# Performance work log

Hardware: AMD Instinct MI355X
Metric: run time of the kernel (lower is better)

Reference implementation:

```python
import jax, jax.numpy as jnp
import numpy as np

NUM_QUANTIZERS = 8


def setup_inputs() -> dict:
    key = jax.random.key(0)
    k1, k2 = jax.random.split(key)
    B, W, C = 16, 2048, 512
    Q, K = NUM_QUANTIZERS, 1024
    x = jax.random.normal(k1, (B, W, C), dtype=jnp.float32)
    # per-stage codebooks (shared_codebook=False), xavier-normal-ish scale
    codebooks = jax.random.normal(k2, (Q, K, C), dtype=jnp.float32) * (2.0 / (K + C)) ** 0.5
    return {"x": x, "codebooks": codebooks}


def reference(x, codebooks):
    """Residual quantization: per-stage cdist+argmin+lookup+residual update.

    x: [B, W, C] encoder latents; codebooks: [Q, K, C].
    Returns (final_z_q [B*W, C], commitment_loss scalar) — final_z_q is
    sum over quantizer stages of the straight-through quantized outputs
    (is_train=True path).
    """
    B, W, C = x.shape
    first_z_e = x.reshape(B * W, C)            # (b w) c
    z_e = first_z_e
    z_d = jnp.zeros_like(first_z_e)
    quant_sum = jnp.zeros_like(first_z_e)
    q_latent = jnp.float32(0.0)
    e_latent = jnp.float32(0.0)
    rq_latent = jnp.float32(0.0)
    for i in range(codebooks.shape[0]):
        cb = codebooks[i]                      # [K, C]
        # squared euclidean distances (argmin-equivalent to torch.cdist)
        dist2 = (jnp.sum(z_e * z_e, axis=1, keepdims=True)
                 - 2.0 * (z_e @ cb.T)
                 + jnp.sum(cb * cb, axis=1))   # [N, K]
        idx = jnp.argmin(dist2, axis=1)        # [N]
        z_q = cb[idx]                          # codebook lookup, [N, C]
        z_d = z_d + jax.lax.stop_gradient(z_q)
        q_latent = q_latent + jnp.mean((jax.lax.stop_gradient(z_e) - z_q) ** 2)
        e_latent = e_latent + jnp.mean((z_e - jax.lax.stop_gradient(z_q)) ** 2)
        rq_latent = rq_latent + jnp.mean((first_z_e - z_d) ** 2)
        # straight-through estimator (is_train=True)
        z_q_st = z_e + jax.lax.stop_gradient(z_q - z_e)
        quant_sum = quant_sum + z_q_st
        z_e = z_e - z_q_st
    commitment_loss = 0.75 * q_latent + e_latent + rq_latent
    return quant_sum, commitment_loss
```

## Files before the change

kernel.cpp:

```cpp
#include <hip/hip_runtime.h>

#define N_ROWS 32768
#define C_DIM  512
#define K_CODES 1024
#define Q_STAGES 8

typedef __attribute__((ext_vector_type(8))) short bf16x8;
typedef __attribute__((ext_vector_type(4))) float f32x4;
typedef __attribute__((ext_vector_type(4))) unsigned short u16x4;
typedef __attribute__((ext_vector_type(8))) unsigned short u16x8;

#define ZEH_OFF 0ull
#define ZEL_OFF 33554432ull
#define CBH_OFF 67108864ull
#define CBL_OFF 68157440ull
#define C2_OFF  69206016ull
#define IDX_OFF 69238784ull
#define RPT_OFF 69304320ull

#define GLD(gp, lp) __builtin_amdgcn_global_load_lds( \
    (const __attribute__((address_space(1))) void*)(gp), \
    (__attribute__((address_space(3))) void*)(lp), 16, 0, 0)

__device__ __forceinline__ float bf_hi_f(float f) {
    return __uint_as_float(__float_as_uint(f) & 0xFFFF0000u);
}
__device__ __forceinline__ unsigned short bf_hi_u(float f) {
    return (unsigned short)(__float_as_uint(f) >> 16);
}
__device__ __forceinline__ float u2f(unsigned short u) {
    return __uint_as_float(((unsigned int)u) << 16);
}

__global__ __launch_bounds__(256) void split_kernel(
    const float* __restrict__ src, unsigned short* __restrict__ h,
    unsigned short* __restrict__ l, int n4)
{
    int i = blockIdx.x * 256 + threadIdx.x;
    if (i >= n4) return;
    float4 v = *(const float4*)(src + (size_t)i * 4);
    u16x4 hv, lv;
    float f, hf;
    f = v.x; hv[0] = bf_hi_u(f); hf = bf_hi_f(f); lv[0] = bf_hi_u(f - hf);
    f = v.y; hv[1] = bf_hi_u(f); hf = bf_hi_f(f); lv[1] = bf_hi_u(f - hf);
    f = v.z; hv[2] = bf_hi_u(f); hf = bf_hi_f(f); lv[2] = bf_hi_u(f - hf);
    f = v.w; hv[3] = bf_hi_u(f); hf = bf_hi_f(f); lv[3] = bf_hi_u(f - hf);
    *(u16x4*)(h + (size_t)i * 4) = hv;
    *(u16x4*)(l + (size_t)i * 4) = lv;
}

__global__ __launch_bounds__(256) void rowsq_kernel(
    const float* __restrict__ src, float* __restrict__ dst, int nrows)
{
    int wave = (blockIdx.x * blockDim.x + threadIdx.x) >> 6;
    int lane = threadIdx.x & 63;
    if (wave >= nrows) return;
    const float* p = src + (size_t)wave * C_DIM + lane * 8;
    float4 a = *(const float4*)p;
    float4 b = *(const float4*)(p + 4);
    float s = a.x*a.x + a.y*a.y + a.z*a.z + a.w*a.w
            + b.x*b.x + b.y*b.y + b.z*b.z + b.w*b.w;
    #pragma unroll
    for (int off = 1; off < 64; off <<= 1) s += __shfl_xor(s, off);
    if (lane == 0) dst[wave] = s;
}

#define DBM2 128
#define DBNC 256
#define DBK 32
#define NSTEPS 64

__global__ __launch_bounds__(512, 2) void dist_kernel(
    const unsigned short* __restrict__ zeh, const unsigned short* __restrict__ zel,
    const unsigned short* __restrict__ cbh, const unsigned short* __restrict__ cbl,
    const float* __restrict__ c2s, unsigned short* __restrict__ idx_out)
{
    __shared__ unsigned short sA[3][2][DBM2 * DBK];
    __shared__ unsigned short sB[3][2][DBNC * DBK];
    __shared__ float c2_lds[K_CODES];

    const int tid  = threadIdx.x;
    const int lane = tid & 63;
    const int w    = tid >> 6;
    const int wr   = w >> 2;
    const int wc   = w & 3;
    const int lr   = lane & 15;
    const int kg   = lane >> 4;
    const int row0 = blockIdx.x * DBM2;

    for (int i = tid; i < K_CODES; i += 512) c2_lds[i] = c2s[i];

    const int srow = lane >> 2;
    const int scol = (((lane & 3) ^ ((srow >> 1) & 3))) * 8;
    const int aslot = (kg ^ ((lr >> 1) & 3)) * 8;

    float rbv[4][4];
    int   rbi[4][4];
    #pragma unroll
    for (int i = 0; i < 4; ++i)
        #pragma unroll
        for (int r = 0; r < 4; ++r) { rbv[i][r] = 3.4e38f; rbi[i][r] = 0x7fffffff; }

    f32x4 acc[4][4];
    #pragma unroll
    for (int i = 0; i < 4; ++i)
        #pragma unroll
        for (int j = 0; j < 4; ++j) acc[i][j] = (f32x4)0.f;

    auto stage = [&](int t, int b) {
        const int col0 = (t >> 4) * DBNC;
        const int kk = (t & 15) * DBK;
        GLD(zeh + (size_t)(row0 + w * 16 + srow) * C_DIM + kk + scol,
            &sA[b][0][(w * 16) * DBK]);
        GLD(zel + (size_t)(row0 + w * 16 + srow) * C_DIM + kk + scol,
            &sA[b][1][(w * 16) * DBK]);
        #pragma unroll
        for (int u = 0; u < 2; ++u) {
            const int rB = w * 32 + u * 16;
            GLD(cbh + (size_t)(col0 + rB + srow) * C_DIM + kk + scol,
                &sB[b][0][rB * DBK]);
            GLD(cbl + (size_t)(col0 + rB + srow) * C_DIM + kk + scol,
                &sB[b][1][rB * DBK]);
        }
    };

    __syncthreads();
    stage(0, 0);
    stage(1, 1);

    int cur = 0;
    #pragma unroll 1
    for (int t = 0; t < NSTEPS; ++t) {
        if (t == NSTEPS - 1) {
            asm volatile("s_waitcnt vmcnt(0)" ::: "memory");
        } else {
            asm volatile("s_waitcnt vmcnt(6)" ::: "memory");
        }
        __builtin_amdgcn_s_barrier();

        bf16x8 ah[4], al[4], bh[4], bl[4];
        #pragma unroll
        for (int mi = 0; mi < 4; ++mi) {
            const int rowoff = (wr * 64 + mi * 16 + lr) * DBK + aslot;
            ah[mi] = *(const bf16x8*)&sA[cur][0][rowoff];
            al[mi] = *(const bf16x8*)&sA[cur][1][rowoff];
        }
        #pragma unroll
        for (int ni = 0; ni < 4; ++ni) {
            const int rowoff = (wc * 64 + ni * 16 + lr) * DBK + aslot;
            bh[ni] = *(const bf16x8*)&sB[cur][0][rowoff];
            bl[ni] = *(const bf16x8*)&sB[cur][1][rowoff];
        }

        if (t < NSTEPS - 2) {
            int nxt = cur + 2; if (nxt > 2) nxt -= 3;
            stage(t + 2, nxt);
        }

        __builtin_amdgcn_s_setprio(1);
        #pragma unroll
        for (int mi = 0; mi < 4; ++mi)
            #pragma unroll
            for (int ni = 0; ni < 4; ++ni)
                acc[mi][ni] = __builtin_amdgcn_mfma_f32_16x16x32_bf16(
                    ah[mi], bh[ni], acc[mi][ni], 0, 0, 0);
        #pragma unroll
        for (int mi = 0; mi < 4; ++mi)
            #pragma unroll
            for (int ni = 0; ni < 4; ++ni)
                acc[mi][ni] = __builtin_amdgcn_mfma_f32_16x16x32_bf16(
                    ah[mi], bl[ni], acc[mi][ni], 0, 0, 0);
        #pragma unroll
        for (int mi = 0; mi < 4; ++mi)
            #pragma unroll
            for (int ni = 0; ni < 4; ++ni)
                acc[mi][ni] = __builtin_amdgcn_mfma_f32_16x16x32_bf16(
                    al[mi], bh[ni], acc[mi][ni], 0, 0, 0);
        __builtin_amdgcn_s_setprio(0);

        if ((t & 15) == 15) {
            const int col0 = (t >> 4) * DBNC;
            #pragma unroll
            for (int ni = 0; ni < 4; ++ni) {
                const int code = col0 + wc * 64 + ni * 16 + lr;
                const float c2v = c2_lds[code];
                #pragma unroll
                for (int mi = 0; mi < 4; ++mi)
                    #pragma unroll
                    for (int r = 0; r < 4; ++r) {
                        float d = fmaf(-2.f, acc[mi][ni][r], c2v);
                        if (d < rbv[mi][r]) { rbv[mi][r] = d; rbi[mi][r] = code; }
                    }
            }
            #pragma unroll
            for (int i = 0; i < 4; ++i)
                #pragma unroll
                for (int j = 0; j < 4; ++j) acc[i][j] = (f32x4)0.f;
        }

        cur = (cur == 2) ? 0 : cur + 1;
    }

    #pragma unroll
    for (int off = 1; off < 16; off <<= 1) {
        #pragma unroll
        for (int mi = 0; mi < 4; ++mi)
            #pragma unroll
            for (int r = 0; r < 4; ++r) {
                float ov = __shfl_xor(rbv[mi][r], off);
                int   oi = __shfl_xor(rbi[mi][r], off);
                if (ov < rbv[mi][r] || (ov == rbv[mi][r] && oi < rbi[mi][r])) {
                    rbv[mi][r] = ov; rbi[mi][r] = oi;
                }
            }
    }

    __syncthreads();
    float (*s_v)[4] = (float (*)[4])&sA[0][0][0];
    int   (*s_i)[4] = (int (*)[4])((char*)&sA[0][0][0] + DBM2 * 4 * 4);
    if (lr == 0) {
        #pragma unroll
        for (int mi = 0; mi < 4; ++mi)
            #pragma unroll
            for (int r = 0; r < 4; ++r) {
                int lrow = wr * 64 + mi * 16 + kg * 4 + r;
                s_v[lrow][wc] = rbv[mi][r];
                s_i[lrow][wc] = rbi[mi][r];
            }
    }
    __syncthreads();
    if (tid < DBM2) {
        float bv = s_v[tid][0]; int bi = s_i[tid][0];
        #pragma unroll
        for (int c = 1; c < 4; ++c) {
            float v = s_v[tid][c]; int i = s_i[tid][c];
            if (v < bv || (v == bv && i < bi)) { bv = v; bi = i; }
        }
        idx_out[row0 + tid] = (unsigned short)bi;
    }
}

__global__ __launch_bounds__(1024) void update_kernel(
    const int s, const float* __restrict__ x, const float* __restrict__ cb,
    const float* __restrict__ cb_next, const unsigned short* __restrict__ idx_sel,
    float* __restrict__ out, unsigned short* __restrict__ zeh,
    unsigned short* __restrict__ zel, unsigned short* __restrict__ cbh,
    unsigned short* __restrict__ cbl, float* __restrict__ rpart)
{
    if (blockIdx.x >= 2048) {
        int i = (blockIdx.x - 2048) * 1024 + threadIdx.x;
        float4 v = *(const float4*)(cb_next + (size_t)i * 4);
        u16x4 hv, lv;
        float f, hf;
        f = v.x; hv[0] = bf_hi_u(f); hf = bf_hi_f(f); lv[0] = bf_hi_u(f - hf);
        f = v.y; hv[1] = bf_hi_u(f); hf = bf_hi_f(f); lv[1] = bf_hi_u(f - hf);
        f = v.z; hv[2] = bf_hi_u(f); hf = bf_hi_f(f); lv[2] = bf_hi_u(f - hf);
        f = v.w; hv[3] = bf_hi_u(f); hf = bf_hi_f(f); lv[3] = bf_hi_u(f - hf);
        *(u16x4*)(cbh + (size_t)i * 4) = hv;
        *(u16x4*)(cbl + (size_t)i * 4) = lv;
        return;
    }

    __shared__ float swsum[16];
    const int wid = threadIdx.x >> 6, lane = threadIdx.x & 63;
    const int r = blockIdx.x * 16 + wid;
    const int bi = idx_sel[r];
    const size_t base = (size_t)r * C_DIM + lane * 8;
    const float* q = cb + (size_t)bi * C_DIM + lane * 8;

    float4 q0 = *(const float4*)q;
    float4 q1 = *(const float4*)(q + 4);
    float qq[8] = {q0.x, q0.y, q0.z, q0.w, q1.x, q1.y, q1.z, q1.w};

    float v[8];
    if (s == 0) {
        float4 z0 = *(const float4*)(x + base);
        float4 z1 = *(const float4*)(x + base + 4);
        v[0]=z0.x; v[1]=z0.y; v[2]=z0.z; v[3]=z0.w;
        v[4]=z1.x; v[5]=z1.y; v[6]=z1.z; v[7]=z1.w;
    } else {
        u16x8 h = *(const u16x8*)(zeh + base);
        u16x8 l = *(const u16x8*)(zel + base);
        #pragma unroll
        for (int j = 0; j < 8; ++j) v[j] = u2f(h[j]) + u2f(l[j]);
    }

    float rr[8];
    #pragma unroll
    for (int j = 0; j < 8; ++j) rr[j] = v[j] - qq[j];

    if (s < Q_STAGES - 1) {
        u16x8 hh, ll;
        #pragma unroll
        for (int j = 0; j < 8; ++j) {
            hh[j] = bf_hi_u(rr[j]);
            float lo = rr[j] - bf_hi_f(rr[j]);
            ll[j] = bf_hi_u(lo);
        }
        *(u16x8*)(zeh + base) = hh;
        *(u16x8*)(zel + base) = ll;
    } else {
        float4 x0 = *(const float4*)(x + base);
        float4 x1 = *(const float4*)(x + base + 4);
        float4 o0, o1;
        o0.x = x0.x - rr[0]; o0.y = x0.y - rr[1];
        o0.z = x0.z - rr[2]; o0.w = x0.w - rr[3];
        o1.x = x1.x - rr[4]; o1.y = x1.y - rr[5];
        o1.z = x1.z - rr[6]; o1.w = x1.w - rr[7];
        *(float4*)(out + base)     = o0;
        *(float4*)(out + base + 4) = o1;
    }

    float ssum = 0.f;
    #pragma unroll
    for (int j = 0; j < 8; ++j) ssum += rr[j] * rr[j];
    #pragma unroll
    for (int off = 1; off < 64; off <<= 1) ssum += __shfl_xor(ssum, off);
    if (lane == 0) swsum[wid] = ssum;
    __syncthreads();
    if (threadIdx.x == 0) {
        float t = 0.f;
        #pragma unroll
        for (int i = 0; i < 16; ++i) t += swsum[i];
        rpart[blockIdx.x] = t;
    }
}

__global__ __launch_bounds__(1024) void finalize_all_kernel(
    const float* __restrict__ rpart, float* __restrict__ out_loss)
{
    __shared__ float sm[1024];
    const int t = threadIdx.x;
    float tot = 0.f;
    for (int s = 0; s < Q_STAGES; ++s) {
        sm[t] = rpart[s * 2048 + t] + rpart[s * 2048 + 1024 + t];
        __syncthreads();
        for (int w2 = 512; w2 > 0; w2 >>= 1) {
            if (t < w2) sm[t] += sm[t + w2];
            __syncthreads();
        }
        if (t == 0) tot += sm[0];
        __syncthreads();
    }
    if (t == 0) out_loss[0] = 2.75f * tot / (float)((size_t)N_ROWS * C_DIM);
}

extern "C" void kernel_launch(void* const* d_in, const int* in_sizes, int n_in,
                              void* d_out, int out_size, void* d_ws, size_t ws_size,
                              hipStream_t stream)
{
    const float* x   = (const float*)d_in[0];
    const float* cbs = (const float*)d_in[1];
    float* out = (float*)d_out;
    char* ws = (char*)d_ws;

    unsigned short* zeh = (unsigned short*)(ws + ZEH_OFF);
    unsigned short* zel = (unsigned short*)(ws + ZEL_OFF);
    unsigned short* cbh = (unsigned short*)(ws + CBH_OFF);
    unsigned short* cbl = (unsigned short*)(ws + CBL_OFF);
    float* c2    = (float*)(ws + C2_OFF);
    unsigned short* gidx = (unsigned short*)(ws + IDX_OFF);
    float* rpart = (float*)(ws + RPT_OFF);

    split_kernel<<<(N_ROWS * C_DIM / 4 + 255) / 256, 256, 0, stream>>>(
        x, zeh, zel, N_ROWS * C_DIM / 4);
    split_kernel<<<(K_CODES * C_DIM / 4 + 255) / 256, 256, 0, stream>>>(
        cbs, cbh, cbl, K_CODES * C_DIM / 4);
    rowsq_kernel<<<(Q_STAGES * K_CODES * 64) / 256, 256, 0, stream>>>(
        cbs, c2, Q_STAGES * K_CODES);

    for (int s = 0; s < Q_STAGES; ++s) {
        const float* cb  = cbs + (size_t)s * K_CODES * C_DIM;
        const float* cbn = (s < Q_STAGES - 1) ? cb + (size_t)K_CODES * C_DIM : cbs;
        dist_kernel<<<N_ROWS / DBM2, 512, 0, stream>>>(
            zeh, zel, cbh, cbl, c2 + (size_t)s * K_CODES, gidx);
        const int nblk = (s < Q_STAGES - 1) ? 2048 + 128 : 2048;
        update_kernel<<<nblk, 1024, 0, stream>>>(
            s, x, cb, cbn, gidx, out, zeh, zel, cbh, cbl, rpart + s * 2048);
    }
    finalize_all_kernel<<<1, 1024, 0, stream>>>(rpart, out + (size_t)N_ROWS * C_DIM);
}
```

Baseline: 988.2 us.

## Load codebook fragments straight into registers and double-buffer the latent tiles

The codebook (B operand) tile no longer goes through LDS. Each wave loads its own MFMA B fragments directly from global memory into double-buffered registers, one step ahead. The latent (A) tile now uses two LDS buffers with a one-step prefetch instead of three buffers with a two-step prefetch. This removes LDS traffic and footprint for B, but waves sharing a column slice load the same codebook data twice. It also relies on short-row strided global reads and only one step of latency hiding.

Measured after the change: 1.503 ms. +52.1%, slower.

```diff
diff --git a/kernel.cpp b/kernel.cpp
--- a/kernel.cpp
+++ b/kernel.cpp
@@ -70,13 +70,87 @@
 #define DBK 32
 #define NSTEPS 64
 
+#define STAGE_A(t, b) do {                                                  \
+    const int kk_ = ((t) & 15) * DBK;                                       \
+    GLD(zeh + (size_t)(row0 + w * 16 + srow) * C_DIM + kk_ + scol,          \
+        &sA[b][0][(w * 16) * DBK]);                                         \
+    GLD(zel + (size_t)(row0 + w * 16 + srow) * C_DIM + kk_ + scol,          \
+        &sA[b][1][(w * 16) * DBK]);                                         \
+} while (0)
+
+#define LOAD_B(t, bh_, bl_) do {                                            \
+    const size_t o_ = bofs + (size_t)((t) >> 4) * (DBNC * C_DIM)            \
+                    + ((t) & 15) * DBK;                                     \
+    _Pragma("unroll")                                                       \
+    for (int ni_ = 0; ni_ < 4; ++ni_) {                                     \
+        bh_[ni_] = *(const bf16x8*)(cbh + o_ + ni_ * 16 * C_DIM);           \
+        bl_[ni_] = *(const bf16x8*)(cbl + o_ + ni_ * 16 * C_DIM);           \
+    }                                                                       \
+} while (0)
+
+#define STEP(t, ab, bhC, blC, bhN, blN) do {                                \
+    asm volatile("s_waitcnt vmcnt(8)" ::: "memory");                        \
+    __builtin_amdgcn_s_barrier();                                           \
+    bf16x8 ah_[4], al_[4];                                                  \
+    _Pragma("unroll")                                                       \
+    for (int mi_ = 0; mi_ < 4; ++mi_) {                                     \
+        const int ro_ = (wr * 64 + mi_ * 16 + lr) * DBK + aslot;            \
+        ah_[mi_] = *(const bf16x8*)&sA[ab][0][ro_];                         \
+        al_[mi_] = *(const bf16x8*)&sA[ab][1][ro_];                         \
+    }                                                                       \
+    if ((t) < NSTEPS - 1) {                                                 \
+        STAGE_A((t) + 1, (ab) ^ 1);                                         \
+        LOAD_B((t) + 1, bhN, blN);                                          \
+    }                                                                       \
+    __builtin_amdgcn_s_setprio(1);                                          \
+    _Pragma("unroll")                                                       \
+    for (int mi_ = 0; mi_ < 4; ++mi_)                                       \
+        _Pragma("unroll")                                                   \
+        for (int ni_ = 0; ni_ < 4; ++ni_)                                   \
+            acc[mi_][ni_] = __builtin_amdgcn_mfma_f32_16x16x32_bf16(        \
+                ah_[mi_], bhC[ni_], acc[mi_][ni_], 0, 0, 0);                \
+    _Pragma("unroll")                                                       \
+    for (int mi_ = 0; mi_ < 4; ++mi_)                                       \
+        _Pragma("unroll")                                                   \
+        for (int ni_ = 0; ni_ < 4; ++ni_)                                   \
+            acc[mi_][ni_] = __builtin_amdgcn_mfma_f32_16x16x32_bf16(        \
+                ah_[mi_], blC[ni_], acc[mi_][ni_], 0, 0, 0);                \
+    _Pragma("unroll")                                                       \
+    for (int mi_ = 0; mi_ < 4; ++mi_)                                       \
+        _Pragma("unroll")                                                   \
+        for (int ni_ = 0; ni_ < 4; ++ni_)                                   \
+            acc[mi_][ni_] = __builtin_amdgcn_mfma_f32_16x16x32_bf16(        \
+                al_[mi_], bhC[ni_], acc[mi_][ni_], 0, 0, 0);                \
+    __builtin_amdgcn_s_setprio(0);                                          \
+    if (((t) & 15) == 15) {                                                 \
+        const int col0_ = ((t) >> 4) * DBNC;                                \
+        _Pragma("unroll")                                                   \
+        for (int ni_ = 0; ni_ < 4; ++ni_) {                                 \
+            const int code_ = col0_ + wc * 64 + ni_ * 16 + lr;              \
+            const float c2v_ = c2_lds[code_];                               \
+            _Pragma("unroll")                                               \
+            for (int mi_ = 0; mi_ < 4; ++mi_)                               \
+                _Pragma("unroll")                                           \
+                for (int r_ = 0; r_ < 4; ++r_) {                            \
+                    float d_ = fmaf(-2.f, acc[mi_][ni_][r_], c2v_);         \
+                    if (d_ < rbv[mi_][r_]) {                                \
+                        rbv[mi_][r_] = d_; rbi[mi_][r_] = code_;            \
+                    }                                                       \
+                }                                                           \
+        }                                                                   \
+        _Pragma("unroll")                                                   \
+        for (int i_ = 0; i_ < 4; ++i_)                                      \
+            _Pragma("unroll")                                               \
+            for (int j_ = 0; j_ < 4; ++j_) acc[i_][j_] = (f32x4)0.f;        \
+    }                                                                       \
+} while (0)
+
 __global__ __launch_bounds__(512, 2) void dist_kernel(
     const unsigned short* __restrict__ zeh, const unsigned short* __restrict__ zel,
     const unsigned short* __restrict__ cbh, const unsigned short* __restrict__ cbl,
     const float* __restrict__ c2s, unsigned short* __restrict__ idx_out)
 {
-    __shared__ unsigned short sA[3][2][DBM2 * DBK];
-    __shared__ unsigned short sB[3][2][DBNC * DBK];
+    __shared__ unsigned short sA[2][2][DBM2 * DBK];
     __shared__ float c2_lds[K_CODES];
 
     const int tid  = threadIdx.x;
@@ -94,6 +168,8 @@
     const int scol = (((lane & 3) ^ ((srow >> 1) & 3))) * 8;
     const int aslot = (kg ^ ((lr >> 1) & 3)) * 8;
 
+    const size_t bofs = (size_t)(wc * 64 + lr) * C_DIM + kg * 8;
+
     float rbv[4][4];
     int   rbi[4][4];
     #pragma unroll
@@ -107,98 +183,17 @@
         #pragma unroll
         for (int j = 0; j < 4; ++j) acc[i][j] = (f32x4)0.f;
 
-    auto stage = [&](int t, int b) {
-        const int col0 = (t >> 4) * DBNC;
-        const int kk = (t & 15) * DBK;
-        GLD(zeh + (size_t)(row0 + w * 16 + srow) * C_DIM + kk + scol,
-            &sA[b][0][(w * 16) * DBK]);
-        GLD(zel + (size_t)(row0 + w * 16 + srow) * C_DIM + kk + scol,
-            &sA[b][1][(w * 16) * DBK]);
-        #pragma unroll
-        for (int u = 0; u < 2; ++u) {
-            const int rB = w * 32 + u * 16;
-            GLD(cbh + (size_t)(col0 + rB + srow) * C_DIM + kk + scol,
-                &sB[b][0][rB * DBK]);
-            GLD(cbl + (size_t)(col0 + rB + srow) * C_DIM + kk + scol,
-                &sB[b][1][rB * DBK]);
-        }
-    };
-
     __syncthreads();
-    stage(0, 0);
-    stage(1, 1);
-
-    int cur = 0;
+
+    STAGE_A(0, 0);
+    bf16x8 bhA[4], blA[4], bhB[4], blB[4];
+    LOAD_B(0, bhA, blA);
+
     #pragma unroll 1
-    for (int t = 0; t < NSTEPS; ++t) {
-        if (t == NSTEPS - 1) {
-            asm volatile("s_waitcnt vmcnt(0)" ::: "memory");
-        } else {
-            asm volatile("s_waitcnt vmcnt(6)" ::: "memory");
-        }
-        __builtin_amdgcn_s_barrier();
-
-        bf16x8 ah[4], al[4], bh[4], bl[4];
-        #pragma unroll
-        for (int mi = 0; mi < 4; ++mi) {
-            const int rowoff = (wr * 64 + mi * 16 + lr) * DBK + aslot;
-            ah[mi] = *(const bf16x8*)&sA[cur][0][rowoff];
-            al[mi] = *(const bf16x8*)&sA[cur][1][rowoff];
-        }
-        #pragma unroll
-        for (int ni = 0; ni < 4; ++ni) {
-            const int rowoff = (wc * 64 + ni * 16 + lr) * DBK + aslot;
-            bh[ni] = *(const bf16x8*)&sB[cur][0][rowoff];
-            bl[ni] = *(const bf16x8*)&sB[cur][1][rowoff];
-        }
-
-        if (t < NSTEPS - 2) {
-            int nxt = cur + 2; if (nxt > 2) nxt -= 3;
-            stage(t + 2, nxt);
-        }
-
-        __builtin_amdgcn_s_setprio(1);
-        #pragma unroll
-        for (int mi = 0; mi < 4; ++mi)
-            #pragma unroll
-            for (int ni = 0; ni < 4; ++ni)
-                acc[mi][ni] = __builtin_amdgcn_mfma_f32_16x16x32_bf16(
-                    ah[mi], bh[ni], acc[mi][ni], 0, 0, 0);
-        #pragma unroll
-        for (int mi = 0; mi < 4; ++mi)
-            #pragma unroll
-            for (int ni = 0; ni < 4; ++ni)
-                acc[mi][ni] = __builtin_amdgcn_mfma_f32_16x16x32_bf16(
-                    ah[mi], bl[ni], acc[mi][ni], 0, 0, 0);
-        #pragma unroll
-        for (int mi = 0; mi < 4; ++mi)
-            #pragma unroll
-            for (int ni = 0; ni < 4; ++ni)
-                acc[mi][ni] = __builtin_amdgcn_mfma_f32_16x16x32_bf16(
-                    al[mi], bh[ni], acc[mi][ni], 0, 0, 0);
-        __builtin_amdgcn_s_setprio(0);
-
-        if ((t & 15) == 15) {
-            const int col0 = (t >> 4) * DBNC;
-            #pragma unroll
-            for (int ni = 0; ni < 4; ++ni) {
-                const int code = col0 + wc * 64 + ni * 16 + lr;
-                const float c2v = c2_lds[code];
-                #pragma unroll
-                for (int mi = 0; mi < 4; ++mi)
-                    #pragma unroll
-                    for (int r = 0; r < 4; ++r) {
-                        float d = fmaf(-2.f, acc[mi][ni][r], c2v);
-                        if (d < rbv[mi][r]) { rbv[mi][r] = d; rbi[mi][r] = code; }
-                    }
-            }
-            #pragma unroll
-            for (int i = 0; i < 4; ++i)
-                #pragma unroll
-                for (int j = 0; j < 4; ++j) acc[i][j] = (f32x4)0.f;
-        }
-
-        cur = (cur == 2) ? 0 : cur + 1;
+    for (int i = 0; i < NSTEPS / 2; ++i) {
+        const int t0 = 2 * i;
+        STEP(t0,     0, bhA, blA, bhB, blB);
+        STEP(t0 + 1, 1, bhB, blB, bhA, blA);
     }
 
     #pragma unroll
```

## Widen dist kernel code tile to 512 and switch to double buffering

Applied to the files above, without the earlier changes.

The distance GEMM's code-column tile doubles from 256 to 512, so each wave holds a 4x8 accumulator tile and the K loop runs half as many steps. The staging pipeline drops from triple to double buffering with a full vmcnt(0) wait each step. The B operand hi/lo fragments are loaded in two phases to limit register use, and c2 is read straight from global memory instead of LDS. The intent is more MFMA work per LDS byte and fewer passes over z_e. The risks are much higher register pressure (128 accumulator floats) under launch_bounds(512,2), possible spills, and less latency hiding from the shallower pipeline.

Result: slower. 1.082 ms (+9.5%).

```diff
diff --git a/kernel.cpp b/kernel.cpp
--- a/kernel.cpp
+++ b/kernel.cpp
@@ -66,18 +66,17 @@
 }
 
 #define DBM2 128
-#define DBNC 256
+#define DBNC2 512
 #define DBK 32
-#define NSTEPS 64
+#define NSTEPS 32
 
 __global__ __launch_bounds__(512, 2) void dist_kernel(
     const unsigned short* __restrict__ zeh, const unsigned short* __restrict__ zel,
     const unsigned short* __restrict__ cbh, const unsigned short* __restrict__ cbl,
     const float* __restrict__ c2s, unsigned short* __restrict__ idx_out)
 {
-    __shared__ unsigned short sA[3][2][DBM2 * DBK];
-    __shared__ unsigned short sB[3][2][DBNC * DBK];
-    __shared__ float c2_lds[K_CODES];
+    __shared__ unsigned short sA[2][2][DBM2 * DBK];
+    __shared__ unsigned short sB[2][2][DBNC2 * DBK];
 
     const int tid  = threadIdx.x;
     const int lane = tid & 63;
@@ -88,8 +87,6 @@
     const int kg   = lane >> 4;
     const int row0 = blockIdx.x * DBM2;
 
-    for (int i = tid; i < K_CODES; i += 512) c2_lds[i] = c2s[i];
-
     const int srow = lane >> 2;
     const int scol = (((lane & 3) ^ ((srow >> 1) & 3))) * 8;
     const int aslot = (kg ^ ((lr >> 1) & 3)) * 8;
@@ -101,22 +98,22 @@
         #pragma unroll
         for (int r = 0; r < 4; ++r) { rbv[i][r] = 3.4e38f; rbi[i][r] = 0x7fffffff; }
 
-    f32x4 acc[4][4];
+    f32x4 acc[4][8];
     #pragma unroll
     for (int i = 0; i < 4; ++i)
         #pragma unroll
-        for (int j = 0; j < 4; ++j) acc[i][j] = (f32x4)0.f;
+        for (int j = 0; j < 8; ++j) acc[i][j] = (f32x4)0.f;
 
     auto stage = [&](int t, int b) {
-        const int col0 = (t >> 4) * DBNC;
+        const int col0 = (t >> 4) * DBNC2;
         const int kk = (t & 15) * DBK;
         GLD(zeh + (size_t)(row0 + w * 16 + srow) * C_DIM + kk + scol,
             &sA[b][0][(w * 16) * DBK]);
         GLD(zel + (size_t)(row0 + w * 16 + srow) * C_DIM + kk + scol,
             &sA[b][1][(w * 16) * DBK]);
         #pragma unroll
-        for (int u = 0; u < 2; ++u) {
-            const int rB = w * 32 + u * 16;
+        for (int u = 0; u < 4; ++u) {
+            const int rB = w * 64 + u * 16;
             GLD(cbh + (size_t)(col0 + rB + srow) * C_DIM + kk + scol,
                 &sB[b][0][rB * DBK]);
             GLD(cbl + (size_t)(col0 + rB + srow) * C_DIM + kk + scol,
@@ -124,66 +121,65 @@
         }
     };
 
-    __syncthreads();
     stage(0, 0);
-    stage(1, 1);
-
-    int cur = 0;
+
     #pragma unroll 1
     for (int t = 0; t < NSTEPS; ++t) {
-        if (t == NSTEPS - 1) {
-            asm volatile("s_waitcnt vmcnt(0)" ::: "memory");
-        } else {
-            asm volatile("s_waitcnt vmcnt(6)" ::: "memory");
-        }
+        const int cur = t & 1;
+        asm volatile("s_waitcnt vmcnt(0)" ::: "memory");
         __builtin_amdgcn_s_barrier();
 
-        bf16x8 ah[4], al[4], bh[4], bl[4];
+        if (t < NSTEPS - 1) stage(t + 1, cur ^ 1);
+
+        bf16x8 ah[4], al[4], bx[8];
         #pragma unroll
         for (int mi = 0; mi < 4; ++mi) {
-            const int rowoff = (wr * 64 + mi * 16 + lr) * DBK + aslot;
-            ah[mi] = *(const bf16x8*)&sA[cur][0][rowoff];
-            al[mi] = *(const bf16x8*)&sA[cur][1][rowoff];
-        }
-        #pragma unroll
-        for (int ni = 0; ni < 4; ++ni) {
-            const int rowoff = (wc * 64 + ni * 16 + lr) * DBK + aslot;
-            bh[ni] = *(const bf16x8*)&sB[cur][0][rowoff];
-            bl[ni] = *(const bf16x8*)&sB[cur][1][rowoff];
-        }
-
-        if (t < NSTEPS - 2) {
-            int nxt = cur + 2; if (nxt > 2) nxt -= 3;
-            stage(t + 2, nxt);
+            const int ro = (wr * 64 + mi * 16 + lr) * DBK + aslot;
+            ah[mi] = *(const bf16x8*)&sA[cur][0][ro];
+            al[mi] = *(const bf16x8*)&sA[cur][1][ro];
+        }
+        #pragma unroll
+        for (int ni = 0; ni < 8; ++ni) {
+            const int ro = (wc * 128 + ni * 16 + lr) * DBK + aslot;
+            bx[ni] = *(const bf16x8*)&sB[cur][0][ro];
         }
 
         __builtin_amdgcn_s_setprio(1);
         #pragma unroll
         for (int mi = 0; mi < 4; ++mi)
             #pragma unroll
-            for (int ni = 0; ni < 4; ++ni)
+            for (int ni = 0; ni < 8; ++ni)
                 acc[mi][ni] = __builtin_amdgcn_mfma_f32_16x16x32_bf16(
-                    ah[mi], bh[ni], acc[mi][ni], 0, 0, 0);
-        #pragma unroll
-        for (int mi = 0; mi < 4; ++mi)
-            #pragma unroll
-            for (int ni = 0; ni < 4; ++ni)
+                    ah[mi], bx[ni], acc[mi][ni], 0, 0, 0);
+        #pragma unroll
+        for (int mi = 0; mi < 4; ++mi)
+            #pragma unroll
+            for (int ni = 0; ni < 8; ++ni)
                 acc[mi][ni] = __builtin_amdgcn_mfma_f32_16x16x32_bf16(
-                    ah[mi], bl[ni], acc[mi][ni], 0, 0, 0);
-        #pragma unroll
-        for (int mi = 0; mi < 4; ++mi)
-            #pragma unroll
-            for (int ni = 0; ni < 4; ++ni)
+                    al[mi], bx[ni], acc[mi][ni], 0, 0, 0);
+        __builtin_amdgcn_s_setprio(0);
+
+        #pragma unroll
+        for (int ni = 0; ni < 8; ++ni) {
+            const int ro = (wc * 128 + ni * 16 + lr) * DBK + aslot;
+            bx[ni] = *(const bf16x8*)&sB[cur][1][ro];
+        }
+
+        __builtin_amdgcn_s_setprio(1);
+        #pragma unroll
+        for (int mi = 0; mi < 4; ++mi)
+            #pragma unroll
+            for (int ni = 0; ni < 8; ++ni)
                 acc[mi][ni] = __builtin_amdgcn_mfma_f32_16x16x32_bf16(
-                    al[mi], bh[ni], acc[mi][ni], 0, 0, 0);
+                    ah[mi], bx[ni], acc[mi][ni], 0, 0, 0);
         __builtin_amdgcn_s_setprio(0);
 
         if ((t & 15) == 15) {
-            const int col0 = (t >> 4) * DBNC;
-            #pragma unroll
-            for (int ni = 0; ni < 4; ++ni) {
-                const int code = col0 + wc * 64 + ni * 16 + lr;
-                const float c2v = c2_lds[code];
+            const int col0 = (t >> 4) * DBNC2;
+            #pragma unroll
+            for (int ni = 0; ni < 8; ++ni) {
+                const int code = col0 + wc * 128 + ni * 16 + lr;
+                const float c2v = c2s[code];
                 #pragma unroll
                 for (int mi = 0; mi < 4; ++mi)
                     #pragma unroll
@@ -195,10 +191,8 @@
             #pragma unroll
             for (int i = 0; i < 4; ++i)
                 #pragma unroll
-                for (int j = 0; j < 4; ++j) acc[i][j] = (f32x4)0.f;
-        }
-
-        cur = (cur == 2) ? 0 : cur + 1;
+                for (int j = 0; j < 8; ++j) acc[i][j] = (f32x4)0.f;
+        }
     }
 
     #pragma unroll
```

## Shrink distance tile to 64 rows with 4 waves and double buffering

Applied to the files above, without the earlier changes.

The distance GEMM block goes from 128x256 with 8 waves and triple-buffered LDS to 64x256 with 4 waves and double buffering. The prefetch is issued right after the barrier with a full vmcnt(0) wait, and the per-block c2 LDS preload is dropped in favour of reading c2 from global memory during the argmin epilogue. This halves the LDS footprint per block and doubles the grid size, which may allow more concurrent blocks. In exchange, codebook tiles are reused across half as many rows, so codebook global traffic doubles, and the shallower pipeline exposes more load latency.

Result: slower. 1.139 ms (+15.2%).

```diff
diff --git a/kernel.cpp b/kernel.cpp
--- a/kernel.cpp
+++ b/kernel.cpp
@@ -65,30 +65,25 @@
     if (lane == 0) dst[wave] = s;
 }
 
-#define DBM2 128
+#define DBM3 64
 #define DBNC 256
 #define DBK 32
 #define NSTEPS 64
 
-__global__ __launch_bounds__(512, 2) void dist_kernel(
+__global__ __launch_bounds__(256, 2) void dist_kernel(
     const unsigned short* __restrict__ zeh, const unsigned short* __restrict__ zel,
     const unsigned short* __restrict__ cbh, const unsigned short* __restrict__ cbl,
     const float* __restrict__ c2s, unsigned short* __restrict__ idx_out)
 {
-    __shared__ unsigned short sA[3][2][DBM2 * DBK];
-    __shared__ unsigned short sB[3][2][DBNC * DBK];
-    __shared__ float c2_lds[K_CODES];
+    __shared__ unsigned short sA[2][2][DBM3 * DBK];
+    __shared__ unsigned short sB[2][2][DBNC * DBK];
 
     const int tid  = threadIdx.x;
     const int lane = tid & 63;
     const int w    = tid >> 6;
-    const int wr   = w >> 2;
-    const int wc   = w & 3;
     const int lr   = lane & 15;
     const int kg   = lane >> 4;
-    const int row0 = blockIdx.x * DBM2;
-
-    for (int i = tid; i < K_CODES; i += 512) c2_lds[i] = c2s[i];
+    const int row0 = blockIdx.x * DBM3;
 
     const int srow = lane >> 2;
     const int scol = (((lane & 3) ^ ((srow >> 1) & 3))) * 8;
@@ -115,8 +110,8 @@
         GLD(zel + (size_t)(row0 + w * 16 + srow) * C_DIM + kk + scol,
             &sA[b][1][(w * 16) * DBK]);
         #pragma unroll
-        for (int u = 0; u < 2; ++u) {
-            const int rB = w * 32 + u * 16;
+        for (int u = 0; u < 4; ++u) {
+            const int rB = w * 64 + u * 16;
             GLD(cbh + (size_t)(col0 + rB + srow) * C_DIM + kk + scol,
                 &sB[b][0][rB * DBK]);
             GLD(cbl + (size_t)(col0 + rB + srow) * C_DIM + kk + scol,
@@ -124,37 +119,28 @@
         }
     };
 
-    __syncthreads();
     stage(0, 0);
-    stage(1, 1);
-
-    int cur = 0;
+
     #pragma unroll 1
     for (int t = 0; t < NSTEPS; ++t) {
-        if (t == NSTEPS - 1) {
-            asm volatile("s_waitcnt vmcnt(0)" ::: "memory");
-        } else {
-            asm volatile("s_waitcnt vmcnt(6)" ::: "memory");
-        }
+        const int cur = t & 1;
+        asm volatile("s_waitcnt vmcnt(0)" ::: "memory");
         __builtin_amdgcn_s_barrier();
 
+        if (t < NSTEPS - 1) stage(t + 1, cur ^ 1);
+
         bf16x8 ah[4], al[4], bh[4], bl[4];
         #pragma unroll
         for (int mi = 0; mi < 4; ++mi) {
-            const int rowoff = (wr * 64 + mi * 16 + lr) * DBK + aslot;
-            ah[mi] = *(const bf16x8*)&sA[cur][0][rowoff];
-            al[mi] = *(const bf16x8*)&sA[cur][1][rowoff];
+            const int ro = (mi * 16 + lr) * DBK + aslot;
+            ah[mi] = *(const bf16x8*)&sA[cur][0][ro];
+            al[mi] = *(const bf16x8*)&sA[cur][1][ro];
         }
         #pragma unroll
         for (int ni = 0; ni < 4; ++ni) {
-            const int rowoff = (wc * 64 + ni * 16 + lr) * DBK + aslot;
-            bh[ni] = *(const bf16x8*)&sB[cur][0][rowoff];
-            bl[ni] = *(const bf16x8*)&sB[cur][1][rowoff];
-        }
-
-        if (t < NSTEPS - 2) {
-            int nxt = cur + 2; if (nxt > 2) nxt -= 3;
-            stage(t + 2, nxt);
+            const int ro = (w * 64 + ni * 16 + lr) * DBK + aslot;
+            bh[ni] = *(const bf16x8*)&sB[cur][0][ro];
+            bl[ni] = *(const bf16x8*)&sB[cur][1][ro];
         }
 
         __builtin_amdgcn_s_setprio(1);
@@ -182,8 +168,8 @@
             const int col0 = (t >> 4) * DBNC;
             #pragma unroll
             for (int ni = 0; ni < 4; ++ni) {
-                const int code = col0 + wc * 64 + ni * 16 + lr;
-                const float c2v = c2_lds[code];
+                const int code = col0 + w * 64 + ni * 16 + lr;
+                const float c2v = c2s[code];
                 #pragma unroll
                 for (int mi = 0; mi < 4; ++mi)
                     #pragma unroll
@@ -197,8 +183,6 @@
                 #pragma unroll
                 for (int j = 0; j < 4; ++j) acc[i][j] = (f32x4)0.f;
         }
-
-        cur = (cur == 2) ? 0 : cur + 1;
     }
 
     #pragma unroll
@@ -217,19 +201,19 @@
 
     __syncthreads();
     float (*s_v)[4] = (float (*)[4])&sA[0][0][0];
-    int   (*s_i)[4] = (int (*)[4])((char*)&sA[0][0][0] + DBM2 * 4 * 4);
+    int   (*s_i)[4] = (int (*)[4])((char*)&sA[0][0][0] + DBM3 * 4 * 4);
     if (lr == 0) {
         #pragma unroll
         for (int mi = 0; mi < 4; ++mi)
             #pragma unroll
             for (int r = 0; r < 4; ++r) {
-                int lrow = wr * 64 + mi * 16 + kg * 4 + r;
-                s_v[lrow][wc] = rbv[mi][r];
-                s_i[lrow][wc] = rbi[mi][r];
+                int lrow = mi * 16 + kg * 4 + r;
+                s_v[lrow][w] = rbv[mi][r];
+                s_i[lrow][w] = rbi[mi][r];
             }
     }
     __syncthreads();
-    if (tid < DBM2) {
+    if (tid < DBM3) {
         float bv = s_v[tid][0]; int bi = s_i[tid][0];
         #pragma unroll
         for (int c = 1; c < 4; ++c) {
@@ -372,7 +356,7 @@
     for (int s = 0; s < Q_STAGES; ++s) {
         const float* cb  = cbs + (size_t)s * K_CODES * C_DIM;
         const float* cbn = (s < Q_STAGES - 1) ? cb + (size_t)K_CODES * C_DIM : cbs;
-        dist_kernel<<<N_ROWS / DBM2, 512, 0, stream>>>(
+        dist_kernel<<<N_ROWS / DBM3, 256, 0, stream>>>(
             zeh, zel, cbh, cbl, c2 + (size_t)s * K_CODES, gidx);
         const int nblk = (s < Q_STAGES - 1) ? 2048 + 128 : 2048;
         update_kernel<<<nblk, 1024, 0, stream>>>(
```
